# Kernel tuning notes

Hardware: AMD Instinct MI355X
Metric: run time of the kernel (lower is better)

The kernel has to match this reference:

```python
import jax, jax.numpy as jnp
import numpy as np

N, E, F, H, EA = 50000, 500000, 2000, 128, 2
NUM_BOND_TYPES = 100
COORDS_RANGE = 10.0
NORM_FACTOR = 100.0


def setup_inputs() -> dict:
    key = jax.random.key(0)
    ks = jax.random.split(key, 20)

    def lin(k, i, o, gain=1.0):
        # xavier-uniform-ish init, stored as [in, out] so forward is x @ W + b
        lim = gain * np.sqrt(6.0 / (i + o))
        return jax.random.uniform(k, (i, o), jnp.float32, -lim, lim)

    inp = {
        "h_a": jax.random.normal(ks[0], (N, H), jnp.float32),
        "x_a": jax.random.normal(ks[1], (N, 3), jnp.float32),
        "e_a_idx": jax.random.randint(ks[2], (2, E), 0, N),
        "e_a_type": jax.random.randint(ks[3], (E,), 0, NUM_BOND_TYPES),
        "e_a_attr": jax.random.normal(ks[4], (E, EA), jnp.float32),
        "coord_diff_a": jax.random.normal(ks[5], (E, 3), jnp.float32),
        "h_f": jax.random.normal(ks[6], (F, H), jnp.float32),
        "x_f": jax.random.normal(ks[7], (F, 3), jnp.float32),
        "bm_mat": jax.random.normal(ks[8], (N, F), jnp.float32) / np.sqrt(F),
        # parameters
        "bond_emb": jax.random.normal(ks[9], (NUM_BOND_TYPES, H), jnp.float32),
        "aW1": lin(ks[10], 2 * H + EA + H, H), "ab1": jnp.zeros((H,), jnp.float32),
        "aW2": lin(ks[11], H, H), "ab2": jnp.zeros((H,), jnp.float32),
        "aW3": lin(ks[12], H, 1, gain=0.001),  # xavier gain=0.001, no bias
        "fW1": lin(ks[13], 2 * H + EA, H), "fb1": jnp.zeros((H,), jnp.float32),
        "fW2": lin(ks[14], H, H), "fb2": jnp.zeros((H,), jnp.float32),
        "fW3": lin(ks[15], H, 1, gain=0.001),
    }
    return inp


def reference(h_a, x_a, e_a_idx, e_a_type, e_a_attr, coord_diff_a, h_f, x_f, bm_mat,
              bond_emb, aW1, ab1, aW2, ab2, aW3, fW1, fb1, fW2, fb2, fW3):
    silu = jax.nn.silu
    row, col = e_a_idx[0], e_a_idx[1]

    be = bond_emb[e_a_type]                              # [E, H]
    coord_diff_f = x_a - bm_mat @ x_f                    # [N, 3]
    radial_f = jnp.sum(coord_diff_f ** 2, axis=1, keepdims=True)  # [N, 1]
    norm_f = jnp.sqrt(radial_f + 1e-8)
    coord_diff_f = coord_diff_f / (norm_f + 1.0)

    inp_atom = jnp.concatenate([h_a[row], h_a[col], e_a_attr, be], axis=1)        # [E, 3H+2]
    inp_frag = jnp.concatenate([h_a, bm_mat @ h_f, radial_f, radial_f], axis=1)   # [N, 2H+2]

    m_atom = silu(silu(inp_atom @ aW1 + ab1) @ aW2 + ab2) @ aW3  # [E, 1]
    m_frag = silu(silu(inp_frag @ fW1 + fb1) @ fW2 + fb2) @ fW3  # [N, 1]

    trans_atom = coord_diff_a * jnp.tanh(m_atom) * COORDS_RANGE  # [E, 3]
    trans_frag = coord_diff_f * jnp.tanh(m_frag) * COORDS_RANGE  # [N, 3]

    agg_atom = jax.ops.segment_sum(trans_atom, row, num_segments=x_a.shape[0]) / NORM_FACTOR
    return x_a + agg_atom + trans_frag
```

## Files before the change

### kernel.cpp

```cpp
#include <hip/hip_runtime.h>
#include <hip/hip_bf16.h>


typedef __attribute__((ext_vector_type(8))) short bfrag8;
typedef __attribute__((ext_vector_type(16))) float f32x16;
typedef __attribute__((ext_vector_type(4))) float f32x4v;

#define MFMA32(A, B, C) __builtin_amdgcn_mfma_f32_32x32x16_bf16((A), (B), (C), 0, 0, 0)

__device__ __forceinline__ f32x16 zero16() {
  f32x16 v;
#pragma unroll
  for (int i = 0; i < 16; ++i) v[i] = 0.0f;
  return v;
}

__device__ __forceinline__ unsigned short bf16bits(float x) {
  __hip_bfloat16 b = __float2bfloat16(x);
  unsigned short u;
  __builtin_memcpy(&u, &b, 2);
  return u;
}

__device__ __forceinline__ unsigned pk2(float lo, float hi) {
  return (unsigned)bf16bits(lo) | ((unsigned)bf16bits(hi) << 16);
}

__device__ __forceinline__ bfrag8 ldfrag(const unsigned short* p) {
  return *reinterpret_cast<const bfrag8*>(p);
}

__device__ __forceinline__ bfrag8 frag4(unsigned f0, unsigned f1, unsigned f2, unsigned f3) {
  union { unsigned u[4]; bfrag8 v; } q;
  q.u[0] = f0; q.u[1] = f1; q.u[2] = f2; q.u[3] = f3;
  return q.v;
}

__device__ __forceinline__ float silu_f(float x) { return x / (1.0f + __expf(-x)); }

__global__ __launch_bounds__(256) void prep_kernel(
    const float* __restrict__ h_a, const float* __restrict__ bond,
    const float* __restrict__ h_f,
    const float* __restrict__ aW1, const float* __restrict__ ab1,
    const float* __restrict__ aW2,
    const float* __restrict__ fW1, const float* __restrict__ fW2,
    unsigned short* __restrict__ h_bf, unsigned short* __restrict__ bond_bf,
    float* __restrict__ hfp,
    unsigned short* __restrict__ W1aT, unsigned short* __restrict__ W1bT,
    unsigned short* __restrict__ W1cT, unsigned short* __restrict__ W1eT,
    unsigned short* __restrict__ W2T,
    unsigned short* __restrict__ fW1aT, unsigned short* __restrict__ fW2T,
    float* __restrict__ agg,
    int N, int NB, int F) {
  const int t = threadIdx.x;
  int bid = blockIdx.x;
  const int G_A = (N * 16 + 255) >> 8;
  const int G_B = (NB * 16 + 255) >> 8;
  const int G_H = (F + 1) >> 1;

  if (bid < G_A + G_B) {
    const float* src = (bid < G_A) ? h_a : bond;
    unsigned short* dst = (bid < G_A) ? h_bf : bond_bf;
    int rows = (bid < G_A) ? N : NB;
    int idx = (bid < G_A ? bid : bid - G_A) * 256 + t;
    if (idx < rows * 16) {
      int row = idx >> 4, g = idx & 15;
      int h = g & 1, kc = g >> 1;
      const f32x4v* s = reinterpret_cast<const f32x4v*>(src + (size_t)row * 128 + g * 8);
      f32x4v v0 = s[0], v1 = s[1];
      unsigned* d = reinterpret_cast<unsigned*>(dst + (size_t)row * 128 + h * 64 + kc * 8);
      d[0] = pk2(v0[0], v0[1]);
      d[1] = pk2(v0[2], v0[3]);
      d[2] = pk2(v1[0], v1[1]);
      d[3] = pk2(v1[2], v1[3]);
    }
    return;
  }
  bid -= G_A + G_B;
  if (bid < G_H) {
    int f = bid * 2 + (t >> 7), n = t & 127;
    if (f < F) {
      float acc = 0.0f;
#pragma unroll 8
      for (int k = 0; k < 128; ++k)
        acc += h_f[(size_t)f * 128 + k] * fW1[(size_t)(128 + k) * 128 + n];
      hfp[(size_t)f * 128 + n] = acc;
    }
    return;
  }
  bid -= G_H;
  if (bid < 6 * 64) {
    int p = bid >> 6;
    int tt = (bid & 63) * 256 + t;
    int j = tt & 7, l = (tt >> 3) & 63, rem = tt >> 9;
    int nt = rem & 3, kc = rem >> 2;
    int k = kc * 16 + ((l >> 5) << 3) + j;
    int n = nt * 32 + (l & 31);
    const float* W;
    unsigned short* D;
    switch (p) {
      case 0: W = aW1;             D = W1aT;  break;
      case 1: W = aW1 + 128 * 128; D = W1bT;  break;
      case 2: W = aW1 + 258 * 128; D = W1cT;  break;
      case 3: W = aW2;             D = W2T;   break;
      case 4: W = fW1;             D = fW1aT; break;
      default: W = fW2;            D = fW2T;  break;
    }
    D[tt] = bf16bits(W[(size_t)k * 128 + n]);
    return;
  }
  bid -= 6 * 64;
  if (bid < 8) {
    int tt = bid * 256 + t;
    if (tt < 4 * 64 * 8) {
      int j = tt & 7, l = (tt >> 3) & 63, nt = (tt >> 9) & 3;
      int k = ((l >> 5) << 3) + j;
      int n = nt * 32 + (l & 31);
      float v = (k == 0) ? aW1[(size_t)256 * 128 + n]
              : (k == 1) ? aW1[(size_t)257 * 128 + n]
              : (k == 2) ? ab1[n] : 0.0f;
      W1eT[tt] = bf16bits(v);
    }
    return;
  }
  bid -= 8;
  {
    int i4 = (bid * 256 + t) * 4;
    if (i4 + 3 < N * 3) {
      *reinterpret_cast<f32x4v*>(agg + i4) = f32x4v{0.f, 0.f, 0.f, 0.f};
    } else {
      for (int c = 0; c < 4; ++c)
        if (i4 + c < N * 3) agg[i4 + c] = 0.0f;
    }
  }
}

__global__ void pack_bmat_kernel(const float* __restrict__ hfp, const float* __restrict__ x_f,
                                 unsigned short* __restrict__ dst, int total) {
  int t = blockIdx.x * blockDim.x + threadIdx.x;
  if (t >= total) return;
  int j = t & 7, l = (t >> 3) & 63, rem = t >> 9;
  int nt = rem % 5, kc = rem / 5;
  int k = kc * 16 + ((l >> 5) << 3) + j;
  int n = nt * 32 + (l & 31);
  float v;
  if (n < 128) v = hfp[(size_t)k * 128 + n];
  else if (n < 131) v = x_f[(size_t)k * 3 + (n - 128)];
  else v = 0.0f;
  dst[t] = bf16bits(v);
}

__global__ __launch_bounds__(512, 1) void k1_gemm(
    const float* __restrict__ bm, const unsigned short* __restrict__ bmT,
    float* __restrict__ k1T, int N, int F) {
  __shared__ __align__(16) char lds[2][256 * 128];
  const int t = threadIdx.x;
  const int lane = t & 63;
  const int w = t >> 6;
  const int h = lane >> 5;
  const int ln = lane & 31;
  const int m0 = blockIdx.x * 256;
  const int NT = (F + 63) >> 6;

  f32x16 acc[5];
#pragma unroll
  for (int i = 0; i < 5; ++i) acc[i] = zero16();

  int srow[8], sch[8];
  const float* sptr[8];
#pragma unroll
  for (int p = 0; p < 8; ++p) {
    int c = p * 512 + t;
    srow[p] = c >> 4;
    sch[p] = c & 15;
    int gr = m0 + srow[p];
    if (gr >= N) gr = N - 1;
    sptr[p] = bm + (size_t)gr * F;
  }

  const int myrow = w * 32 + ln;
  const int rsw = (myrow & 7) << 4;

  f32x4v sregs[8];
#pragma unroll
  for (int p = 0; p < 8; ++p) {
    int gk = sch[p] * 4;
    if (gk > F - 4) gk = F - 4;
    sregs[p] = *reinterpret_cast<const f32x4v*>(sptr[p] + gk);
  }
#pragma unroll
  for (int p = 0; p < 8; ++p) {
    int byte = srow[p] * 128 + ((sch[p] * 8) ^ ((srow[p] & 7) << 4));
    union { unsigned u[2]; unsigned long long ull; } q;
    q.u[0] = pk2(sregs[p][0], sregs[p][1]);
    q.u[1] = pk2(sregs[p][2], sregs[p][3]);
    *reinterpret_cast<unsigned long long*>(&lds[0][byte]) = q.ull;
  }
  __syncthreads();

  int cur = 0;
  for (int kt = 0; kt < NT; ++kt) {
    const bool more = (kt + 1 < NT);
    if (more) {
#pragma unroll
      for (int p = 0; p < 8; ++p) {
        int gk = (kt + 1) * 64 + sch[p] * 4;
        if (gk > F - 4) gk = F - 4;
        sregs[p] = *reinterpret_cast<const f32x4v*>(sptr[p] + gk);
      }
    }
    const int kcCount = ((F - kt * 64) >> 4) < 4 ? ((F - kt * 64) >> 4) : 4;
    for (int kc = 0; kc < kcCount; ++kc) {
      bfrag8 b = *reinterpret_cast<const bfrag8*>(
          &lds[cur][myrow * 128 + ((kc * 32 + h * 16) ^ rsw)]);
      const int kcg = kt * 4 + kc;
      const unsigned short* wp = bmT + ((size_t)kcg * 5 * 64 + lane) * 8;
#pragma unroll
      for (int nt = 0; nt < 5; ++nt) acc[nt] = MFMA32(ldfrag(wp + nt * 512), b, acc[nt]);
    }
    if (more) {
#pragma unroll
      for (int p = 0; p < 8; ++p) {
        int byte = srow[p] * 128 + ((sch[p] * 8) ^ ((srow[p] & 7) << 4));
        union { unsigned u[2]; unsigned long long ull; } q;
        q.u[0] = pk2(sregs[p][0], sregs[p][1]);
        q.u[1] = pk2(sregs[p][2], sregs[p][3]);
        *reinterpret_cast<unsigned long long*>(&lds[cur ^ 1][byte]) = q.ull;
      }
    }
    __syncthreads();
    cur ^= 1;
  }

  const int m = m0 + myrow;
  if (m < N) {
#pragma unroll
    for (int nt = 0; nt < 5; ++nt)
#pragma unroll
      for (int r = 0; r < 16; ++r) {
        int n = nt * 32 + (r & 3) + 8 * (r >> 2) + 4 * h;
        if (n < 131) k1T[(size_t)n * N + m] = acc[nt][r];
      }
  }
}

__global__ __launch_bounds__(256) void k3_atom(
    const unsigned short* __restrict__ h_bf, const unsigned short* __restrict__ bond_bf,
    const int* __restrict__ eidx, const int* __restrict__ etype,
    const float* __restrict__ eattr, const float* __restrict__ cda,
    const unsigned short* __restrict__ W1aT, const unsigned short* __restrict__ W1bT,
    const unsigned short* __restrict__ W1cT, const unsigned short* __restrict__ W1eT,
    const unsigned short* __restrict__ W2T,
    const float* __restrict__ ab2, const float* __restrict__ aW3,
    float* __restrict__ agg, int E) {
  const int lane = threadIdx.x & 63;
  const int wid = threadIdx.x >> 6;
  const int h = lane >> 5;
  const int ln = lane & 31;
  const int e = blockIdx.x * 128 + wid * 32 + ln;
  const bool valid = (e < E);
  const int ec = valid ? e : (E - 1);
  const int row = eidx[ec];
  const int col = eidx[(size_t)E + ec];
  const int typ = etype[ec];
  const float e0 = eattr[2 * (size_t)ec];
  const float e1 = eattr[2 * (size_t)ec + 1];

  const unsigned short* hr = h_bf + (size_t)row * 128 + h * 64;
  const unsigned short* hc = h_bf + (size_t)col * 128 + h * 64;
  const unsigned short* bb = bond_bf + (size_t)typ * 128 + h * 64;

  f32x16 acc[4];
#pragma unroll
  for (int q = 0; q < 4; ++q) acc[q] = zero16();

#pragma unroll
  for (int kc = 0; kc < 8; ++kc) {
    bfrag8 b = ldfrag(hr + kc * 8);
    const unsigned short* wp = W1aT + ((size_t)(kc * 4) * 64 + lane) * 8;
#pragma unroll
    for (int nt = 0; nt < 4; ++nt) acc[nt] = MFMA32(ldfrag(wp + nt * 512), b, acc[nt]);
  }
#pragma unroll
  for (int kc = 0; kc < 8; ++kc) {
    bfrag8 b = ldfrag(hc + kc * 8);
    const unsigned short* wp = W1bT + ((size_t)(kc * 4) * 64 + lane) * 8;
#pragma unroll
    for (int nt = 0; nt < 4; ++nt) acc[nt] = MFMA32(ldfrag(wp + nt * 512), b, acc[nt]);
  }
#pragma unroll
  for (int kc = 0; kc < 8; ++kc) {
    bfrag8 b = ldfrag(bb + kc * 8);
    const unsigned short* wp = W1cT + ((size_t)(kc * 4) * 64 + lane) * 8;
#pragma unroll
    for (int nt = 0; nt < 4; ++nt) acc[nt] = MFMA32(ldfrag(wp + nt * 512), b, acc[nt]);
  }
  {
    unsigned u0 = h ? 0u : pk2(e0, e1);
    unsigned u1 = h ? 0u : 0x00003F80u;
    bfrag8 b = frag4(u0, u1, 0u, 0u);
    const unsigned short* wp = W1eT + (size_t)lane * 8;
#pragma unroll
    for (int nt = 0; nt < 4; ++nt) acc[nt] = MFMA32(ldfrag(wp + nt * 512), b, acc[nt]);
  }

  unsigned w[32];
#pragma unroll
  for (int nt = 0; nt < 4; ++nt)
#pragma unroll
    for (int p = 0; p < 8; ++p)
      w[nt * 8 + p] = pk2(silu_f(acc[nt][2 * p]), silu_f(acc[nt][2 * p + 1]));

#pragma unroll
  for (int q = 0; q < 4; ++q) acc[q] = zero16();
#pragma unroll
  for (int kc = 0; kc < 8; ++kc) {
    const int base = (kc >> 1) * 8 + (kc & 1) * 4;
    unsigned a0 = w[base + 0], a1 = w[base + 1], a2 = w[base + 2], a3 = w[base + 3];
    unsigned s0 = (unsigned)__shfl_xor((int)a0, 32);
    unsigned s1 = (unsigned)__shfl_xor((int)a1, 32);
    unsigned s2 = (unsigned)__shfl_xor((int)a2, 32);
    unsigned s3 = (unsigned)__shfl_xor((int)a3, 32);
    bfrag8 b = frag4(h ? s2 : a0, h ? s3 : a1, h ? a2 : s0, h ? a3 : s1);
    const unsigned short* wp = W2T + ((size_t)(kc * 4) * 64 + lane) * 8;
#pragma unroll
    for (int nt = 0; nt < 4; ++nt) acc[nt] = MFMA32(ldfrag(wp + nt * 512), b, acc[nt]);
  }

  float part = 0.0f;
#pragma unroll
  for (int nt = 0; nt < 4; ++nt)
#pragma unroll
    for (int r = 0; r < 16; ++r) {
      int n = nt * 32 + (r & 3) + 8 * (r >> 2) + 4 * h;
      part += silu_f(acc[nt][r] + ab2[n]) * aW3[n];
    }
  float mv = part + __shfl_xor(part, 32);

  if (valid) {
    float tt = tanhf(mv) * 0.1f;
    if (h == 0) {
      atomicAdd(agg + 3 * (size_t)row + 0, cda[3 * (size_t)ec + 0] * tt);
      atomicAdd(agg + 3 * (size_t)row + 1, cda[3 * (size_t)ec + 1] * tt);
    } else {
      atomicAdd(agg + 3 * (size_t)row + 2, cda[3 * (size_t)ec + 2] * tt);
    }
  }
}

__global__ __launch_bounds__(256) void k2_frag(
    const float* __restrict__ x_a, const unsigned short* __restrict__ h_bf,
    const float* __restrict__ k1T, const float* __restrict__ agg,
    const unsigned short* __restrict__ fW1aT, const unsigned short* __restrict__ fW2T,
    const float* __restrict__ fW1, const float* __restrict__ fb1,
    const float* __restrict__ fb2, const float* __restrict__ fW3,
    float* __restrict__ out, int N) {
  const int lane = threadIdx.x & 63;
  const int wid = threadIdx.x >> 6;
  const int h = lane >> 5;
  const int ln = lane & 31;
  const int i = blockIdx.x * 128 + wid * 32 + ln;
  const bool valid = (i < N);
  const int ic = valid ? i : (N - 1);

  float cd[3];
  float radial = 0.0f;
#pragma unroll
  for (int c = 0; c < 3; ++c) {
    float v = x_a[3 * (size_t)ic + c] - k1T[(size_t)(128 + c) * N + ic];
    cd[c] = v;
    radial += v * v;
  }

  f32x16 acc[4];
#pragma unroll
  for (int q = 0; q < 4; ++q) acc[q] = zero16();
  const unsigned short* hp = h_bf + (size_t)ic * 128 + h * 64;
#pragma unroll
  for (int kc = 0; kc < 8; ++kc) {
    bfrag8 b = ldfrag(hp + kc * 8);
    const unsigned short* wp = fW1aT + ((size_t)(kc * 4) * 64 + lane) * 8;
#pragma unroll
    for (int nt = 0; nt < 4; ++nt) acc[nt] = MFMA32(ldfrag(wp + nt * 512), b, acc[nt]);
  }

  unsigned w[32];
#pragma unroll
  for (int nt = 0; nt < 4; ++nt)
#pragma unroll
    for (int p = 0; p < 8; ++p) {
      const int r0 = 2 * p;
      const int n0 = nt * 32 + (r0 & 3) + 8 * (r0 >> 2) + 4 * h;
      const int n1 = n0 + 1;
      float q0 = acc[nt][r0] + k1T[(size_t)n0 * N + ic]
               + radial * (fW1[(size_t)256 * 128 + n0] + fW1[(size_t)257 * 128 + n0]) + fb1[n0];
      float q1 = acc[nt][r0 + 1] + k1T[(size_t)n1 * N + ic]
               + radial * (fW1[(size_t)256 * 128 + n1] + fW1[(size_t)257 * 128 + n1]) + fb1[n1];
      w[nt * 8 + p] = pk2(silu_f(q0), silu_f(q1));
    }

#pragma unroll
  for (int q = 0; q < 4; ++q) acc[q] = zero16();
#pragma unroll
  for (int kc = 0; kc < 8; ++kc) {
    const int base = (kc >> 1) * 8 + (kc & 1) * 4;
    unsigned a0 = w[base + 0], a1 = w[base + 1], a2 = w[base + 2], a3 = w[base + 3];
    unsigned s0 = (unsigned)__shfl_xor((int)a0, 32);
    unsigned s1 = (unsigned)__shfl_xor((int)a1, 32);
    unsigned s2 = (unsigned)__shfl_xor((int)a2, 32);
    unsigned s3 = (unsigned)__shfl_xor((int)a3, 32);
    bfrag8 b = frag4(h ? s2 : a0, h ? s3 : a1, h ? a2 : s0, h ? a3 : s1);
    const unsigned short* wp = fW2T + ((size_t)(kc * 4) * 64 + lane) * 8;
#pragma unroll
    for (int nt = 0; nt < 4; ++nt) acc[nt] = MFMA32(ldfrag(wp + nt * 512), b, acc[nt]);
  }

  float part = 0.0f;
#pragma unroll
  for (int nt = 0; nt < 4; ++nt)
#pragma unroll
    for (int r = 0; r < 16; ++r) {
      int n = nt * 32 + (r & 3) + 8 * (r >> 2) + 4 * h;
      part += silu_f(acc[nt][r] + fb2[n]) * fW3[n];
    }
  float mv = part + __shfl_xor(part, 32);

  if (valid && h == 0) {
    float nrm = sqrtf(radial + 1e-8f);
    float s = tanhf(mv) * 10.0f / (nrm + 1.0f);
#pragma unroll
    for (int c = 0; c < 3; ++c)
      out[3 * (size_t)i + c] = x_a[3 * (size_t)i + c] + cd[c] * s + agg[3 * (size_t)i + c];
  }
}


extern "C" void kernel_launch(void* const* d_in, const int* in_sizes, int n_in,
                              void* d_out, int out_size, void* d_ws, size_t ws_size,
                              hipStream_t stream) {
  const float* h_a    = (const float*)d_in[0];
  const float* x_a    = (const float*)d_in[1];
  const int*   e_idx  = (const int*)d_in[2];
  const int*   e_type = (const int*)d_in[3];
  const float* e_attr = (const float*)d_in[4];
  const float* cda    = (const float*)d_in[5];
  const float* h_f    = (const float*)d_in[6];
  const float* x_f    = (const float*)d_in[7];
  const float* bm     = (const float*)d_in[8];
  const float* bond   = (const float*)d_in[9];
  const float* aW1    = (const float*)d_in[10];
  const float* ab1    = (const float*)d_in[11];
  const float* aW2    = (const float*)d_in[12];
  const float* ab2    = (const float*)d_in[13];
  const float* aW3    = (const float*)d_in[14];
  const float* fW1    = (const float*)d_in[15];
  const float* fb1    = (const float*)d_in[16];
  const float* fW2    = (const float*)d_in[17];
  const float* fb2    = (const float*)d_in[18];
  const float* fW3    = (const float*)d_in[19];
  float* out = (float*)d_out;

  const int N  = in_sizes[0] / 128;
  const int E  = in_sizes[2] / 2;
  const int F  = in_sizes[6] / 128;
  const int NB = in_sizes[9] / 128;
  const int KC = F / 16;

  char* wsp = (char*)d_ws;
  size_t off = 0;
  auto alloc = [&](size_t bytes) -> char* {
    char* p = wsp + off;
    off += (bytes + 255) & ~(size_t)255;
    return p;
  };
  unsigned short* h_bf    = (unsigned short*)alloc((size_t)N * 128 * 2);
  unsigned short* bond_bf = (unsigned short*)alloc((size_t)NB * 128 * 2);
  float*          hfp     = (float*)alloc((size_t)F * 128 * 4);
  unsigned short* bmT     = (unsigned short*)alloc((size_t)KC * 5 * 64 * 8 * 2);
  unsigned short* W1aT    = (unsigned short*)alloc(8 * 4 * 64 * 8 * 2);
  unsigned short* W1bT    = (unsigned short*)alloc(8 * 4 * 64 * 8 * 2);
  unsigned short* W1cT    = (unsigned short*)alloc(8 * 4 * 64 * 8 * 2);
  unsigned short* W2T     = (unsigned short*)alloc(8 * 4 * 64 * 8 * 2);
  unsigned short* fW1aT   = (unsigned short*)alloc(8 * 4 * 64 * 8 * 2);
  unsigned short* fW2T    = (unsigned short*)alloc(8 * 4 * 64 * 8 * 2);
  unsigned short* W1eT    = (unsigned short*)alloc(1 * 4 * 64 * 8 * 2);
  float*          k1T     = (float*)alloc((size_t)131 * N * 4);
  float*          agg     = (float*)alloc((size_t)N * 3 * 4);

  const int G_A = (N * 16 + 255) >> 8;
  const int G_B = (NB * 16 + 255) >> 8;
  const int G_H = (F + 1) >> 1;
  const int G_P = 6 * 64;
  const int G_E2 = 8;
  const int G_Z = (N * 3 + 1023) >> 10;
  prep_kernel<<<G_A + G_B + G_H + G_P + G_E2 + G_Z, 256, 0, stream>>>(
      h_a, bond, h_f, aW1, ab1, aW2, fW1, fW2,
      h_bf, bond_bf, hfp, W1aT, W1bT, W1cT, W1eT, W2T, fW1aT, fW2T, agg,
      N, NB, F);

  {
    int total = KC * 5 * 64 * 8;
    pack_bmat_kernel<<<(total + 255) / 256, 256, 0, stream>>>(hfp, x_f, bmT, total);
  }

  k1_gemm<<<(N + 255) / 256, 512, 0, stream>>>(bm, bmT, k1T, N, F);

  k3_atom<<<(E + 127) / 128, 256, 0, stream>>>(h_bf, bond_bf, e_idx, e_type, e_attr, cda,
                                               W1aT, W1bT, W1cT, W1eT, W2T, ab2, aW3, agg, E);

  k2_frag<<<(N + 127) / 128, 256, 0, stream>>>(x_a, h_bf, k1T, agg, fW1aT, fW2T,
                                               fW1, fb1, fb2, fW3, out, N);
}
```

Measured before the change: 405.8 us.

## Fuse bm GEMM and edge MLP into one launch with block-range dispatch

Merges the dense bm_mat GEMM kernel and the per-edge atom MLP kernel into a single launch. The first G1 blocks run the GEMM and the remaining blocks handle edges, so the two independent workloads can run concurrently on the GPU instead of back to back. The GEMM tile shrinks from 256 to 128 rows with 256-thread blocks and launch bounds allowing two blocks per CU, and the full-tile inner loop is specialised for unrolling. Risks: all edge blocks now reserve the GEMM's shared memory and share its register budget, which can lower occupancy for the edge work, and the smaller GEMM tile reuses bmT less.

```diff
diff --git a/kernel.cpp b/kernel.cpp
--- a/kernel.cpp
+++ b/kernel.cpp
@@ -150,101 +150,9 @@
   dst[t] = bf16bits(v);
 }
 
-__global__ __launch_bounds__(512, 1) void k1_gemm(
+__global__ __launch_bounds__(256, 2) void fused_k1_k3(
     const float* __restrict__ bm, const unsigned short* __restrict__ bmT,
-    float* __restrict__ k1T, int N, int F) {
-  __shared__ __align__(16) char lds[2][256 * 128];
-  const int t = threadIdx.x;
-  const int lane = t & 63;
-  const int w = t >> 6;
-  const int h = lane >> 5;
-  const int ln = lane & 31;
-  const int m0 = blockIdx.x * 256;
-  const int NT = (F + 63) >> 6;
-
-  f32x16 acc[5];
-#pragma unroll
-  for (int i = 0; i < 5; ++i) acc[i] = zero16();
-
-  int srow[8], sch[8];
-  const float* sptr[8];
-#pragma unroll
-  for (int p = 0; p < 8; ++p) {
-    int c = p * 512 + t;
-    srow[p] = c >> 4;
-    sch[p] = c & 15;
-    int gr = m0 + srow[p];
-    if (gr >= N) gr = N - 1;
-    sptr[p] = bm + (size_t)gr * F;
-  }
-
-  const int myrow = w * 32 + ln;
-  const int rsw = (myrow & 7) << 4;
-
-  f32x4v sregs[8];
-#pragma unroll
-  for (int p = 0; p < 8; ++p) {
-    int gk = sch[p] * 4;
-    if (gk > F - 4) gk = F - 4;
-    sregs[p] = *reinterpret_cast<const f32x4v*>(sptr[p] + gk);
-  }
-#pragma unroll
-  for (int p = 0; p < 8; ++p) {
-    int byte = srow[p] * 128 + ((sch[p] * 8) ^ ((srow[p] & 7) << 4));
-    union { unsigned u[2]; unsigned long long ull; } q;
-    q.u[0] = pk2(sregs[p][0], sregs[p][1]);
-    q.u[1] = pk2(sregs[p][2], sregs[p][3]);
-    *reinterpret_cast<unsigned long long*>(&lds[0][byte]) = q.ull;
-  }
-  __syncthreads();
-
-  int cur = 0;
-  for (int kt = 0; kt < NT; ++kt) {
-    const bool more = (kt + 1 < NT);
-    if (more) {
-#pragma unroll
-      for (int p = 0; p < 8; ++p) {
-        int gk = (kt + 1) * 64 + sch[p] * 4;
-        if (gk > F - 4) gk = F - 4;
-        sregs[p] = *reinterpret_cast<const f32x4v*>(sptr[p] + gk);
-      }
-    }
-    const int kcCount = ((F - kt * 64) >> 4) < 4 ? ((F - kt * 64) >> 4) : 4;
-    for (int kc = 0; kc < kcCount; ++kc) {
-      bfrag8 b = *reinterpret_cast<const bfrag8*>(
-          &lds[cur][myrow * 128 + ((kc * 32 + h * 16) ^ rsw)]);
-      const int kcg = kt * 4 + kc;
-      const unsigned short* wp = bmT + ((size_t)kcg * 5 * 64 + lane) * 8;
-#pragma unroll
-      for (int nt = 0; nt < 5; ++nt) acc[nt] = MFMA32(ldfrag(wp + nt * 512), b, acc[nt]);
-    }
-    if (more) {
-#pragma unroll
-      for (int p = 0; p < 8; ++p) {
-        int byte = srow[p] * 128 + ((sch[p] * 8) ^ ((srow[p] & 7) << 4));
-        union { unsigned u[2]; unsigned long long ull; } q;
-        q.u[0] = pk2(sregs[p][0], sregs[p][1]);
-        q.u[1] = pk2(sregs[p][2], sregs[p][3]);
-        *reinterpret_cast<unsigned long long*>(&lds[cur ^ 1][byte]) = q.ull;
-      }
-    }
-    __syncthreads();
-    cur ^= 1;
-  }
-
-  const int m = m0 + myrow;
-  if (m < N) {
-#pragma unroll
-    for (int nt = 0; nt < 5; ++nt)
-#pragma unroll
-      for (int r = 0; r < 16; ++r) {
-        int n = nt * 32 + (r & 3) + 8 * (r >> 2) + 4 * h;
-        if (n < 131) k1T[(size_t)n * N + m] = acc[nt][r];
-      }
-  }
-}
-
-__global__ __launch_bounds__(256) void k3_atom(
+    float* __restrict__ k1T,
     const unsigned short* __restrict__ h_bf, const unsigned short* __restrict__ bond_bf,
     const int* __restrict__ eidx, const int* __restrict__ etype,
     const float* __restrict__ eattr, const float* __restrict__ cda,
@@ -252,12 +160,114 @@
     const unsigned short* __restrict__ W1cT, const unsigned short* __restrict__ W1eT,
     const unsigned short* __restrict__ W2T,
     const float* __restrict__ ab2, const float* __restrict__ aW3,
-    float* __restrict__ agg, int E) {
+    float* __restrict__ agg,
+    int N, int F, int E, int G1) {
+  __shared__ __align__(16) char lds[2][128 * 128];
   const int lane = threadIdx.x & 63;
-  const int wid = threadIdx.x >> 6;
+  const int w = threadIdx.x >> 6;
   const int h = lane >> 5;
   const int ln = lane & 31;
-  const int e = blockIdx.x * 128 + wid * 32 + ln;
+
+  if ((int)blockIdx.x < G1) {
+    const int t = threadIdx.x;
+    const int m0 = blockIdx.x * 128;
+    const int NT = (F + 63) >> 6;
+
+    f32x16 acc[5];
+#pragma unroll
+    for (int i = 0; i < 5; ++i) acc[i] = zero16();
+
+    int srow[8], sch[8];
+    const float* sptr[8];
+#pragma unroll
+    for (int p = 0; p < 8; ++p) {
+      int c = p * 256 + t;
+      srow[p] = c >> 4;
+      sch[p] = c & 15;
+      int gr = m0 + srow[p];
+      if (gr >= N) gr = N - 1;
+      sptr[p] = bm + (size_t)gr * F;
+    }
+
+    const int myrow = w * 32 + ln;
+    const int rsw = (myrow & 7) << 4;
+
+    f32x4v sregs[8];
+#pragma unroll
+    for (int p = 0; p < 8; ++p) {
+      int gk = sch[p] * 4;
+      if (gk > F - 4) gk = F - 4;
+      sregs[p] = *reinterpret_cast<const f32x4v*>(sptr[p] + gk);
+    }
+#pragma unroll
+    for (int p = 0; p < 8; ++p) {
+      int byte = srow[p] * 128 + ((sch[p] * 8) ^ ((srow[p] & 7) << 4));
+      union { unsigned u[2]; unsigned long long ull; } q;
+      q.u[0] = pk2(sregs[p][0], sregs[p][1]);
+      q.u[1] = pk2(sregs[p][2], sregs[p][3]);
+      *reinterpret_cast<unsigned long long*>(&lds[0][byte]) = q.ull;
+    }
+    __syncthreads();
+
+    int cur = 0;
+    for (int kt = 0; kt < NT; ++kt) {
+      const bool more = (kt + 1 < NT);
+      if (more) {
+#pragma unroll
+        for (int p = 0; p < 8; ++p) {
+          int gk = (kt + 1) * 64 + sch[p] * 4;
+          if (gk > F - 4) gk = F - 4;
+          sregs[p] = *reinterpret_cast<const f32x4v*>(sptr[p] + gk);
+        }
+      }
+      const int rem = (F - kt * 64) >> 4;
+      const int kcN = rem < 4 ? rem : 4;
+      if (kcN == 4) {
+#pragma unroll
+        for (int kc = 0; kc < 4; ++kc) {
+          bfrag8 b = *reinterpret_cast<const bfrag8*>(
+              &lds[cur][myrow * 128 + ((kc * 32 + h * 16) ^ rsw)]);
+          const unsigned short* wp = bmT + ((size_t)(kt * 4 + kc) * 5 * 64 + lane) * 8;
+#pragma unroll
+          for (int nt = 0; nt < 5; ++nt) acc[nt] = MFMA32(ldfrag(wp + nt * 512), b, acc[nt]);
+        }
+      } else {
+        for (int kc = 0; kc < kcN; ++kc) {
+          bfrag8 b = *reinterpret_cast<const bfrag8*>(
+              &lds[cur][myrow * 128 + ((kc * 32 + h * 16) ^ rsw)]);
+          const unsigned short* wp = bmT + ((size_t)(kt * 4 + kc) * 5 * 64 + lane) * 8;
+#pragma unroll
+          for (int nt = 0; nt < 5; ++nt) acc[nt] = MFMA32(ldfrag(wp + nt * 512), b, acc[nt]);
+        }
+      }
+      if (more) {
+#pragma unroll
+        for (int p = 0; p < 8; ++p) {
+          int byte = srow[p] * 128 + ((sch[p] * 8) ^ ((srow[p] & 7) << 4));
+          union { unsigned u[2]; unsigned long long ull; } q;
+          q.u[0] = pk2(sregs[p][0], sregs[p][1]);
+          q.u[1] = pk2(sregs[p][2], sregs[p][3]);
+          *reinterpret_cast<unsigned long long*>(&lds[cur ^ 1][byte]) = q.ull;
+        }
+      }
+      __syncthreads();
+      cur ^= 1;
+    }
+
+    const int m = m0 + myrow;
+    if (m < N) {
+#pragma unroll
+      for (int nt = 0; nt < 5; ++nt)
+#pragma unroll
+        for (int r = 0; r < 16; ++r) {
+          int n = nt * 32 + (r & 3) + 8 * (r >> 2) + 4 * h;
+          if (n < 131) k1T[(size_t)n * N + m] = acc[nt][r];
+        }
+    }
+    return;
+  }
+
+  const int e = (blockIdx.x - G1) * 128 + w * 32 + ln;
   const bool valid = (e < E);
   const int ec = valid ? e : (E - 1);
   const int row = eidx[ec];
@@ -304,19 +314,19 @@
     for (int nt = 0; nt < 4; ++nt) acc[nt] = MFMA32(ldfrag(wp + nt * 512), b, acc[nt]);
   }
 
-  unsigned w[32];
+  unsigned wv[32];
 #pragma unroll
   for (int nt = 0; nt < 4; ++nt)
 #pragma unroll
     for (int p = 0; p < 8; ++p)
-      w[nt * 8 + p] = pk2(silu_f(acc[nt][2 * p]), silu_f(acc[nt][2 * p + 1]));
+      wv[nt * 8 + p] = pk2(silu_f(acc[nt][2 * p]), silu_f(acc[nt][2 * p + 1]));
 
 #pragma unroll
   for (int q = 0; q < 4; ++q) acc[q] = zero16();
 #pragma unroll
   for (int kc = 0; kc < 8; ++kc) {
     const int base = (kc >> 1) * 8 + (kc & 1) * 4;
-    unsigned a0 = w[base + 0], a1 = w[base + 1], a2 = w[base + 2], a3 = w[base + 3];
+    unsigned a0 = wv[base + 0], a1 = wv[base + 1], a2 = wv[base + 2], a3 = wv[base + 3];
     unsigned s0 = (unsigned)__shfl_xor((int)a0, 32);
     unsigned s1 = (unsigned)__shfl_xor((int)a1, 32);
     unsigned s2 = (unsigned)__shfl_xor((int)a2, 32);
@@ -384,7 +394,7 @@
     for (int nt = 0; nt < 4; ++nt) acc[nt] = MFMA32(ldfrag(wp + nt * 512), b, acc[nt]);
   }
 
-  unsigned w[32];
+  unsigned wv[32];
 #pragma unroll
   for (int nt = 0; nt < 4; ++nt)
 #pragma unroll
@@ -396,7 +406,7 @@
                + radial * (fW1[(size_t)256 * 128 + n0] + fW1[(size_t)257 * 128 + n0]) + fb1[n0];
       float q1 = acc[nt][r0 + 1] + k1T[(size_t)n1 * N + ic]
                + radial * (fW1[(size_t)256 * 128 + n1] + fW1[(size_t)257 * 128 + n1]) + fb1[n1];
-      w[nt * 8 + p] = pk2(silu_f(q0), silu_f(q1));
+      wv[nt * 8 + p] = pk2(silu_f(q0), silu_f(q1));
     }
 
 #pragma unroll
@@ -404,7 +414,7 @@
 #pragma unroll
   for (int kc = 0; kc < 8; ++kc) {
     const int base = (kc >> 1) * 8 + (kc & 1) * 4;
-    unsigned a0 = w[base + 0], a1 = w[base + 1], a2 = w[base + 2], a3 = w[base + 3];
+    unsigned a0 = wv[base + 0], a1 = wv[base + 1], a2 = wv[base + 2], a3 = wv[base + 3];
     unsigned s0 = (unsigned)__shfl_xor((int)a0, 32);
     unsigned s1 = (unsigned)__shfl_xor((int)a1, 32);
     unsigned s2 = (unsigned)__shfl_xor((int)a2, 32);
@@ -481,9 +491,9 @@
   unsigned short* W1bT    = (unsigned short*)alloc(8 * 4 * 64 * 8 * 2);
   unsigned short* W1cT    = (unsigned short*)alloc(8 * 4 * 64 * 8 * 2);
   unsigned short* W2T     = (unsigned short*)alloc(8 * 4 * 64 * 8 * 2);
+  unsigned short* W1eT    = (unsigned short*)alloc(1 * 4 * 64 * 8 * 2);
   unsigned short* fW1aT   = (unsigned short*)alloc(8 * 4 * 64 * 8 * 2);
   unsigned short* fW2T    = (unsigned short*)alloc(8 * 4 * 64 * 8 * 2);
-  unsigned short* W1eT    = (unsigned short*)alloc(1 * 4 * 64 * 8 * 2);
   float*          k1T     = (float*)alloc((size_t)131 * N * 4);
   float*          agg     = (float*)alloc((size_t)N * 3 * 4);
 
@@ -503,10 +513,13 @@
     pack_bmat_kernel<<<(total + 255) / 256, 256, 0, stream>>>(hfp, x_f, bmT, total);
   }
 
-  k1_gemm<<<(N + 255) / 256, 512, 0, stream>>>(bm, bmT, k1T, N, F);
-
-  k3_atom<<<(E + 127) / 128, 256, 0, stream>>>(h_bf, bond_bf, e_idx, e_type, e_attr, cda,
-                                               W1aT, W1bT, W1cT, W1eT, W2T, ab2, aW3, agg, E);
+  const int G1 = (N + 127) / 128;
+  const int G3 = (E + 127) / 128;
+  fused_k1_k3<<<G1 + G3, 256, 0, stream>>>(
+      bm, bmT, k1T,
+      h_bf, bond_bf, e_idx, e_type, e_attr, cda,
+      W1aT, W1bT, W1cT, W1eT, W2T, ab2, aW3, agg,
+      N, F, E, G1);
 
   k2_frag<<<(N + 127) / 128, 256, 0, stream>>>(x_a, h_bf, k1T, agg, fW1aT, fW2T,
                                                fW1, fb1, fb2, fW3, out, N);
```

Result: faster. 358.5 us (-11.7%).
